# Performance work log

Measured on AMD Instinct MI355X. Metric: run time of the kernel, lower is better.

Reference implementation:

```python
import jax, jax.numpy as jnp
import numpy as np

S = 9                      # spiral length
V = [8192, 4096, 2048, 1024, 512]  # verts per level, finest -> latent


def grid_sample_bilinear(feat, grid):
    # feat [B,C,H,W], grid [B,P,2] in [-1,1]; bilinear, align_corners=True
    B, C, H, W = feat.shape
    x = (grid[..., 0] + 1.0) * 0.5 * (W - 1)
    y = (grid[..., 1] + 1.0) * 0.5 * (H - 1)
    x0 = jnp.floor(x); y0 = jnp.floor(y)
    wx = x - x0; wy = y - y0
    x0i = jnp.clip(x0.astype(jnp.int32), 0, W - 1)
    x1i = jnp.clip(x0.astype(jnp.int32) + 1, 0, W - 1)
    y0i = jnp.clip(y0.astype(jnp.int32), 0, H - 1)
    y1i = jnp.clip(y0.astype(jnp.int32) + 1, 0, H - 1)
    featf = feat.reshape(B, C, H * W).transpose(0, 2, 1)  # [B,HW,C]
    def gat(yi, xi):
        return jnp.take_along_axis(featf, (yi * W + xi)[..., None], axis=1)  # [B,P,C]
    w00 = ((1 - wy) * (1 - wx))[..., None]
    w01 = ((1 - wy) * wx)[..., None]
    w10 = (wy * (1 - wx))[..., None]
    w11 = (wy * wx)[..., None]
    return gat(y0i, x0i) * w00 + gat(y0i, x1i) * w01 + gat(y1i, x0i) * w10 + gat(y1i, x1i) * w11


def pool(x, row, col, val):
    # sparse mesh upsample: gather cols, scale, scatter-add into rows
    n_out = row.shape[0] // 3
    g = x[:, col, :] * val[None, :, None]                       # [B,nnz,C]
    return jnp.zeros((x.shape[0], n_out, x.shape[-1]), x.dtype).at[:, row, :].add(g)


def dsconv(x, idx, wd, wp, b):
    # depthwise-separable spiral conv: gather spiral ring, depthwise over S, pointwise mix
    g = x[:, idx]                                # [B,N,S,C]
    dw = jnp.einsum('bnsc,sc->bnc', g, wd)       # depthwise over spiral dim
    return jnp.einsum('bnc,co->bno', dw, wp) + b # pointwise


def _forward(uv, feat, upsample, s0, s1, s2, s3,
             row0, col0, val0, row1, col1, val1, row2, col2, val2, row3, col3, val3,
             wd0, wp0, b0, wd1, wp1, b1, wd2, wp2, b2, wd3, wp3, b3, wdh, wph, bh):
    uvc = jnp.clip((uv - 0.5) * 2.0, -1.0, 1.0)
    x = grid_sample_bilinear(feat, uvc)           # [B,P,C]  (torch: [B,C,P] then permute)
    x = jnp.einsum('vp,bpc->bvc', upsample, x)    # [B,V4,C] latent mesh features
    x = jax.nn.relu(dsconv(pool(x, row3, col3, val3), s3, wd0, wp0, b0))  # [B,1024,512]
    x = jax.nn.relu(dsconv(pool(x, row2, col2, val2), s2, wd1, wp1, b1))  # [B,2048,256]
    x = jax.nn.relu(dsconv(pool(x, row1, col1, val1), s1, wd2, wp2, b2))  # [B,4096,128]
    x = jax.nn.relu(dsconv(pool(x, row0, col0, val0), s0, wd3, wp3, b3))  # [B,8192,64]
    return dsconv(x, s0, wdh, wph, bh)            # [B,8192,3]


def setup_inputs():
    ks = jax.random.split(jax.random.key(0), 64)
    B, P, C, H, W = 8, 21, 512, 32, 32
    inp = {}
    inp['uv'] = jax.random.uniform(ks[0], (B, P, 2), jnp.float32)
    inp['feat'] = jax.random.normal(ks[1], (B, C, H, W), jnp.float32)
    inp['upsample'] = 0.01 * jnp.ones((V[4], P), jnp.float32)
    for i in range(4):
        inp[f's{i}'] = jax.random.randint(ks[2 + i], (V[i], S), 0, V[i])
    for i in range(4):
        nnz = 3 * V[i]
        inp[f'row{i}'] = jax.random.randint(ks[6 + 3 * i], (nnz,), 0, V[i])
        inp[f'col{i}'] = jax.random.randint(ks[7 + 3 * i], (nnz,), 0, V[i + 1])
        inp[f'val{i}'] = jax.random.uniform(ks[8 + 3 * i], (nnz,), jnp.float32)
    chans = [(512, 512), (512, 256), (256, 128), (128, 64), (64, 3)]
    names = ['0', '1', '2', '3', 'h']
    k = 20
    for (ci, co), nm in zip(chans, names):
        inp[f'wd{nm}'] = 0.1 * jax.random.normal(ks[k], (S, ci), jnp.float32); k += 1
        inp[f'wp{nm}'] = jax.random.normal(ks[k], (ci, co), jnp.float32) * (1.0 / float(np.sqrt(ci))); k += 1
        inp[f'b{nm}'] = jnp.zeros((co,), jnp.float32); k += 1
    return inp


def reference(uv, feat, upsample, s0, s1, s2, s3,
              row0, col0, val0, row1, col1, val1, row2, col2, val2, row3, col3, val3,
              wd0, wp0, b0, wd1, wp1, b1, wd2, wp2, b2, wd3, wp3, b3, wdh, wph, bh):
    return _forward(uv, feat, upsample, s0, s1, s2, s3,
                    row0, col0, val0, row1, col1, val1, row2, col2, val2, row3, col3, val3,
                    wd0, wp0, b0, wd1, wp1, b1, wd2, wp2, b2, wd3, wp3, b3, wdh, wph, bh)
```

## Files before the change

kernel.cpp:

```cpp
#include <hip/hip_runtime.h>

#define B_  8
#define P_  21
#define H_  32
#define W_  32

typedef float f32x4 __attribute__((ext_vector_type(4)));
typedef _Float16 f16x8 __attribute__((ext_vector_type(8)));

__device__ __forceinline__ void gload_lds16(const _Float16* g, _Float16* l) {
  __builtin_amdgcn_global_load_lds(
      (const __attribute__((address_space(1))) void*)g,
      (__attribute__((address_space(3))) void*)l, 16, 0, 0);
}

struct CsrParams {
  const int*   row[4];
  const int*   col[4];
  const float* val[4];
  int*   cnt[4];
  int*   rowptr[4];
  int*   colsout[4];
  float* valsout[4];
  int    nnz[4];
  int    V[4];
};

struct BsplitParams {
  const float* wp[4];
  int K[4], N[4], off[4];
  _Float16* b0;
  _Float16* b1;
};

__global__ __launch_bounds__(256) void k1_zero_sample(
    int* zp, int zn,
    const float* __restrict__ uv,
    const float* __restrict__ feat,
    float* __restrict__ xs) {
  int bid = blockIdx.x;
  if (bid < 60) {
    int i = bid * 256 + threadIdx.x;
    if (i < zn) zp[i] = 0;
    return;
  }
  int bp = bid - 60;
  int b  = bp / P_;
  float u0 = uv[bp * 2 + 0], u1 = uv[bp * 2 + 1];
  float gx = fminf(fmaxf((u0 - 0.5f) * 2.0f, -1.0f), 1.0f);
  float gy = fminf(fmaxf((u1 - 0.5f) * 2.0f, -1.0f), 1.0f);
  float fx = (gx + 1.0f) * 0.5f * (W_ - 1);
  float fy = (gy + 1.0f) * 0.5f * (H_ - 1);
  float x0f = floorf(fx), y0f = floorf(fy);
  float wx = fx - x0f, wy = fy - y0f;
  int x0 = (int)x0f, y0 = (int)y0f;
  int x0i = min(max(x0, 0), W_ - 1), x1i = min(max(x0 + 1, 0), W_ - 1);
  int y0i = min(max(y0, 0), H_ - 1), y1i = min(max(y0 + 1, 0), H_ - 1);
  float w00 = (1.f - wy) * (1.f - wx), w01 = (1.f - wy) * wx;
  float w10 = wy * (1.f - wx),        w11 = wy * wx;
  for (int c = threadIdx.x; c < 512; c += blockDim.x) {
    const float* fb = feat + ((size_t)(b * 512 + c)) * (H_ * W_);
    float v = fb[y0i * W_ + x0i] * w00 + fb[y0i * W_ + x1i] * w01 +
              fb[y1i * W_ + x0i] * w10 + fb[y1i * W_ + x1i] * w11;
    xs[(size_t)bp * 512 + c] = v;
  }
}

__global__ __launch_bounds__(256) void k2_count_upsample(
    CsrParams p,
    const float* __restrict__ up,
    const float* __restrict__ xs,
    float* __restrict__ xu) {
  int bid = blockIdx.x;
  if (bid < 384) {
    int l = bid / 96;
    int k = (bid - l * 96) * 256 + threadIdx.x;
    if (k < p.nnz[l]) atomicAdd(&p.cnt[l][p.row[l][k]], 1);
    return;
  }
  int b2 = bid - 384;
  int b = b2 >> 9, v = b2 & 511;
  int c2 = threadIdx.x << 1;
  float2 acc = make_float2(0.f, 0.f);
  for (int q = 0; q < P_; ++q) {
    float u = up[v * P_ + q];
    const float2 xv = *(const float2*)&xs[((size_t)(b * P_ + q)) * 512 + c2];
    acc.x = fmaf(u, xv.x, acc.x);
    acc.y = fmaf(u, xv.y, acc.y);
  }
  *(float2*)&xu[((size_t)(b * 512 + v)) * 512 + c2] = acc;
}

__global__ __launch_bounds__(256) void k3_scan_bsplit(CsrParams p, BsplitParams bp) {
  int bid = blockIdx.x;
  if (bid < 4) {
    int l = bid;
    int V = p.V[l];
    int* cnt = p.cnt[l];
    int* rp  = p.rowptr[l];
    int t = threadIdx.x;
    int chunk = V / 256;
    int base = t * chunk;
    int s = 0;
    for (int i = 0; i < chunk; ++i) s += cnt[base + i];
    __shared__ int sm[256];
    sm[t] = s;
    __syncthreads();
    for (int off = 1; off < 256; off <<= 1) {
      int v = (t >= off) ? sm[t - off] : 0;
      __syncthreads();
      sm[t] += v;
      __syncthreads();
    }
    int run = sm[t] - s;
    for (int i = 0; i < chunk; ++i) {
      int c = cnt[base + i];
      rp[base + i]  = run;
      cnt[base + i] = run;
      run += c;
    }
    if (t == 255) rp[V] = run;
    return;
  }
  int idx = (bid - 4) * 256 + threadIdx.x;
  #pragma unroll
  for (int t = 0; t < 4; ++t) {
    int sz = bp.N[t] * bp.K[t];
    if (idx < sz) {
      int K = bp.K[t];
      int n = idx / K, k = idx - n * K;
      float v = bp.wp[t][(size_t)k * bp.N[t] + n];
      _Float16 h0 = (_Float16)v;
      float r = (v - (float)h0) * 2048.0f;
      int ks = ((((k >> 3) ^ (n & 7)) << 3) | (k & 7));
      bp.b0[bp.off[t] + (size_t)n * K + ks] = h0;
      bp.b1[bp.off[t] + (size_t)n * K + ks] = (_Float16)r;
      return;
    }
    idx -= sz;
  }
}

__global__ void fill_kernel(CsrParams p) {
  int l = blockIdx.y;
  int k = blockIdx.x * 256 + threadIdx.x;
  if (k < p.nnz[l]) {
    int r = p.row[l][k];
    int pos = atomicAdd(&p.cnt[l][r], 1);
    p.colsout[l][pos] = p.col[l][k];
    p.valsout[l][pos] = p.val[l][k];
  }
}

__global__ __launch_bounds__(256) void pool_kernel(
    const float* __restrict__ x,
    const int* __restrict__ rowptr,
    const int* __restrict__ cols,
    const float* __restrict__ vals,
    float* __restrict__ out,
    int Vout, int Vin, int Cin) {
  const int lpr    = Cin >> 3;
  const int lshift = 31 - __clz(lpr);
  const int rpb    = 256 >> lshift;
  const int lr = threadIdx.x >> lshift;
  const int lc = threadIdx.x & (lpr - 1);
  const int b  = blockIdx.x & 7;
  const int n  = (blockIdx.x >> 3) * rpb + lr;
  const int c8 = lc << 3;
  const float* xb = x + (size_t)b * Vin * Cin + c8;
  int j0 = rowptr[n], j1 = rowptr[n + 1];
  int cnt = j1 - j0;
  float4 a0 = make_float4(0.f, 0.f, 0.f, 0.f);
  float4 a1 = make_float4(0.f, 0.f, 0.f, 0.f);
  if (cnt > 0) {
    int   cc[4];
    float vv[4];
    #pragma unroll
    for (int k = 0; k < 4; ++k) {
      int jj = j0 + ((k < cnt) ? k : 0);
      cc[k] = cols[jj];
      vv[k] = (k < cnt) ? vals[jj] : 0.f;
    }
    #pragma unroll
    for (int k = 0; k < 4; ++k) {
      const float* xr = xb + (size_t)cc[k] * Cin;
      float4 x0 = *(const float4*)xr;
      float4 x1 = *(const float4*)(xr + 4);
      float v = vv[k];
      a0.x = fmaf(v, x0.x, a0.x); a0.y = fmaf(v, x0.y, a0.y);
      a0.z = fmaf(v, x0.z, a0.z); a0.w = fmaf(v, x0.w, a0.w);
      a1.x = fmaf(v, x1.x, a1.x); a1.y = fmaf(v, x1.y, a1.y);
      a1.z = fmaf(v, x1.z, a1.z); a1.w = fmaf(v, x1.w, a1.w);
    }
    for (int j = j0 + 4; j < j1; ++j) {
      float v = vals[j];
      const float* xr = xb + (size_t)cols[j] * Cin;
      float4 x0 = *(const float4*)xr;
      float4 x1 = *(const float4*)(xr + 4);
      a0.x = fmaf(v, x0.x, a0.x); a0.y = fmaf(v, x0.y, a0.y);
      a0.z = fmaf(v, x0.z, a0.z); a0.w = fmaf(v, x0.w, a0.w);
      a1.x = fmaf(v, x1.x, a1.x); a1.y = fmaf(v, x1.y, a1.y);
      a1.z = fmaf(v, x1.z, a1.z); a1.w = fmaf(v, x1.w, a1.w);
    }
  }
  float* op = &out[((size_t)b * Vout + n) * Cin + c8];
  *(float4*)op = a0;
  *(float4*)(op + 4) = a1;
}

__global__ __launch_bounds__(256) void dw_split_kernel(
    const float* __restrict__ xin,
    const int* __restrict__ sidx,
    const float* __restrict__ wd,
    _Float16* __restrict__ a0o,
    _Float16* __restrict__ a1o,
    int Vout, int Cin) {
  const int lpr    = Cin >> 3;
  const int lshift = 31 - __clz(lpr);
  const int rpb    = 256 >> lshift;
  const int lr = threadIdx.x >> lshift;
  const int lc = threadIdx.x & (lpr - 1);
  const int b  = blockIdx.x & 7;
  const int n  = (blockIdx.x >> 3) * rpb + lr;
  const int c8 = lc << 3;
  const float* xb = xin + (size_t)b * Vout * Cin + c8;

  int idx[9];
  #pragma unroll
  for (int s = 0; s < 9; ++s) idx[s] = sidx[n * 9 + s];

  float4 a0 = make_float4(0.f, 0.f, 0.f, 0.f);
  float4 a1 = make_float4(0.f, 0.f, 0.f, 0.f);
  #pragma unroll
  for (int s = 0; s < 9; ++s) {
    const float* xr = xb + (size_t)idx[s] * Cin;
    float4 x0 = *(const float4*)xr;
    float4 x1 = *(const float4*)(xr + 4);
    const float* wr = wd + s * Cin + c8;
    float4 w0 = *(const float4*)wr;
    float4 w1 = *(const float4*)(wr + 4);
    a0.x = fmaf(w0.x, x0.x, a0.x); a0.y = fmaf(w0.y, x0.y, a0.y);
    a0.z = fmaf(w0.z, x0.z, a0.z); a0.w = fmaf(w0.w, x0.w, a0.w);
    a1.x = fmaf(w1.x, x1.x, a1.x); a1.y = fmaf(w1.y, x1.y, a1.y);
    a1.z = fmaf(w1.z, x1.z, a1.z); a1.w = fmaf(w1.w, x1.w, a1.w);
  }

  size_t m = (size_t)b * Vout + n;
  float v[8] = {a0.x, a0.y, a0.z, a0.w, a1.x, a1.y, a1.z, a1.w};
  f16x8 hi, lo;
  #pragma unroll
  for (int i = 0; i < 8; ++i) {
    _Float16 h0 = (_Float16)v[i];
    float r = (v[i] - (float)h0) * 2048.0f;
    hi[i] = h0;
    lo[i] = (_Float16)r;
  }
  const int c8s = (lc ^ (n & 7)) << 3;
  *(f16x8*)&a0o[m * Cin + c8s] = hi;
  *(f16x8*)&a1o[m * Cin + c8s] = lo;
}

__global__ __launch_bounds__(256) void gemm_f16x2(
    const _Float16* __restrict__ A0, const _Float16* __restrict__ A1,
    const _Float16* __restrict__ Bt0, const _Float16* __restrict__ Bt1,
    const float* __restrict__ bias, float* __restrict__ C,
    int M, int N, int K) {
  __shared__ _Float16 As[2][128 * 64];
  __shared__ _Float16 Bs[2][64 * 64];
  const int tid = threadIdx.x;
  const int bx = blockIdx.x;
  const int xr_ = (bx & 7) * (gridDim.x >> 3) + (bx >> 3);
  const int m0 = xr_ * 128, n0 = blockIdx.y * 64;
  const int wid = tid >> 6, lane = tid & 63;
  const int wr = wid >> 1, wc = wid & 1;
  const int lo = lane & 15, hi = lane >> 4;

  f32x4 accM[4][2], accC[4][2];
  #pragma unroll
  for (int mi = 0; mi < 4; ++mi)
    #pragma unroll
    for (int nj = 0; nj < 2; ++nj) {
      accM[mi][nj] = (f32x4){0.f, 0.f, 0.f, 0.f};
      accC[mi][nj] = (f32x4){0.f, 0.f, 0.f, 0.f};
    }

  const _Float16* gA[2] = {A0, A1};
  const _Float16* gB[2] = {Bt0, Bt1};

  for (int k0 = 0; k0 < K; k0 += 64) {
    #pragma unroll
    for (int p = 0; p < 2; ++p) {
      #pragma unroll
      for (int i = 0; i < 4; ++i) {
        int c = tid + 256 * i;
        int r = c >> 3, k8 = (c & 7) << 3;
        gload_lds16(gA[p] + (size_t)(m0 + r) * K + k0 + k8,
                    &As[p][(c & ~63) * 8]);
      }
      #pragma unroll
      for (int i = 0; i < 2; ++i) {
        int c = tid + 256 * i;
        int r = c >> 3, k8 = (c & 7) << 3;
        gload_lds16(gB[p] + (size_t)(n0 + r) * K + k0 + k8,
                    &Bs[p][(c & ~63) * 8]);
      }
    }
    __syncthreads();
    #pragma unroll
    for (int s = 0; s < 2; ++s) {
      const int cl = s * 4 + hi;
      f16x8 af[4][2], bf[2][2];
      #pragma unroll
      for (int mi = 0; mi < 4; ++mi) {
        const int rr = wr * 64 + mi * 16 + lo;
        const int ko = (cl ^ (rr & 7)) << 3;
        af[mi][0] = *(const f16x8*)&As[0][rr * 64 + ko];
        af[mi][1] = *(const f16x8*)&As[1][rr * 64 + ko];
      }
      #pragma unroll
      for (int nj = 0; nj < 2; ++nj) {
        const int rb = wc * 32 + nj * 16 + lo;
        const int ko = (cl ^ (rb & 7)) << 3;
        bf[nj][0] = *(const f16x8*)&Bs[0][rb * 64 + ko];
        bf[nj][1] = *(const f16x8*)&Bs[1][rb * 64 + ko];
      }
      #pragma unroll
      for (int mi = 0; mi < 4; ++mi)
        #pragma unroll
        for (int nj = 0; nj < 2; ++nj) {
          accM[mi][nj] = __builtin_amdgcn_mfma_f32_16x16x32_f16(
              af[mi][0], bf[nj][0], accM[mi][nj], 0, 0, 0);
          accC[mi][nj] = __builtin_amdgcn_mfma_f32_16x16x32_f16(
              af[mi][0], bf[nj][1], accC[mi][nj], 0, 0, 0);
          accC[mi][nj] = __builtin_amdgcn_mfma_f32_16x16x32_f16(
              af[mi][1], bf[nj][0], accC[mi][nj], 0, 0, 0);
        }
    }
    __syncthreads();
  }

  const float INV = 1.0f / 2048.0f;
  #pragma unroll
  for (int mi = 0; mi < 4; ++mi)
    #pragma unroll
    for (int nj = 0; nj < 2; ++nj) {
      int col = n0 + wc * 32 + nj * 16 + lo;
      float bv = bias[col];
      #pragma unroll
      for (int r = 0; r < 4; ++r) {
        int row = m0 + wr * 64 + mi * 16 + hi * 4 + r;
        float v = accM[mi][nj][r] + accC[mi][nj][r] * INV + bv;
        v = fmaxf(v, 0.f);
        C[(size_t)row * N + col] = v;
      }
    }
}

__global__ __launch_bounds__(256) void head_fused_kernel(
    const float* __restrict__ x,
    const int* __restrict__ sidx,
    const float* __restrict__ wdh,
    const float* __restrict__ wph,
    const float* __restrict__ bh,
    float* __restrict__ out) {
  const int bid  = blockIdx.x;
  const int b    = bid & 7;
  const int wid  = threadIdx.x >> 6;
  const int lane = threadIdx.x & 63;
  const int n    = (bid >> 3) * 4 + wid;
  const float* xb = x + (size_t)b * 8192 * 64 + lane;

  int idx[9];
  #pragma unroll
  for (int s = 0; s < 9; ++s) idx[s] = sidx[n * 9 + s];

  float acc = 0.f;
  #pragma unroll
  for (int s = 0; s < 9; ++s)
    acc = fmaf(wdh[s * 64 + lane], xb[(size_t)idx[s] * 64], acc);

  float a0 = acc * wph[lane * 3 + 0];
  float a1 = acc * wph[lane * 3 + 1];
  float a2 = acc * wph[lane * 3 + 2];
  for (int off = 32; off > 0; off >>= 1) {
    a0 += __shfl_down(a0, off);
    a1 += __shfl_down(a1, off);
    a2 += __shfl_down(a2, off);
  }
  if (lane == 0) {
    size_t row = (size_t)b * 8192 + n;
    out[row * 3 + 0] = a0 + bh[0];
    out[row * 3 + 1] = a1 + bh[1];
    out[row * 3 + 2] = a2 + bh[2];
  }
}

extern "C" void kernel_launch(void* const* d_in, const int* in_sizes, int n_in,
                              void* d_out, int out_size, void* d_ws, size_t ws_size,
                              hipStream_t stream) {
  const float* uv   = (const float*)d_in[0];
  const float* feat = (const float*)d_in[1];
  const float* up   = (const float*)d_in[2];
  const int* sArr[4] = {(const int*)d_in[3], (const int*)d_in[4],
                        (const int*)d_in[5], (const int*)d_in[6]};

  const size_t SLAB = 8ull * 2048 * 512;
  float* Wf = (float*)d_ws;
  float* S0 = Wf;
  float* S1 = Wf + SLAB;
  _Float16* A0 = (_Float16*)(S1 + SLAB);
  _Float16* A1 = A0 + SLAB;
  _Float16* Bt0all = (_Float16*)(S0 + 4500000);
  _Float16* Bt1all = Bt0all + 434176;
  float* xs = (float*)(A1 + SLAB);
  int* ib = (int*)(xs + (size_t)B_ * P_ * 512);

  int Vt[4] = {1024, 2048, 4096, 8192};
  int NZ[4] = {3072, 6144, 12288, 24576};
  int* cnt[4]; int* rp[4]; int* co[4]; float* va[4];
  {
    int* pc = ib;
    for (int t = 0; t < 4; ++t) { cnt[t] = pc; pc += Vt[t]; }
    for (int t = 0; t < 4; ++t) { rp[t] = pc; pc += Vt[t] + 1; }
    for (int t = 0; t < 4; ++t) { co[t] = pc; pc += NZ[t]; }
    float* pv = (float*)pc;
    for (int t = 0; t < 4; ++t) { va[t] = pv; pv += NZ[t]; }
  }

  CsrParams cp;
  for (int t = 0; t < 4; ++t) {
    int i = 3 - t;
    cp.row[t] = (const int*)d_in[7 + 3 * i];
    cp.col[t] = (const int*)d_in[8 + 3 * i];
    cp.val[t] = (const float*)d_in[9 + 3 * i];
    cp.cnt[t] = cnt[t]; cp.rowptr[t] = rp[t];
    cp.colsout[t] = co[t]; cp.valsout[t] = va[t];
    cp.nnz[t] = NZ[t]; cp.V[t] = Vt[t];
  }

  struct Stg { int Vin, Vout, Cin, Cout; const int* s; const float *wd, *wp, *bias; };
  Stg st[4] = {
    {512, 1024, 512, 512, sArr[3], (const float*)d_in[19], (const float*)d_in[20], (const float*)d_in[21]},
    {1024, 2048, 512, 256, sArr[2], (const float*)d_in[22], (const float*)d_in[23], (const float*)d_in[24]},
    {2048, 4096, 256, 128, sArr[1], (const float*)d_in[25], (const float*)d_in[26], (const float*)d_in[27]},
    {4096, 8192, 128, 64, sArr[0], (const float*)d_in[28], (const float*)d_in[29], (const float*)d_in[30]},
  };

  BsplitParams bp;
  int boff = 0;
  for (int t = 0; t < 4; ++t) {
    bp.wp[t] = st[t].wp;
    bp.K[t] = st[t].Cin; bp.N[t] = st[t].Cout;
    bp.off[t] = boff;
    boff += st[t].Cin * st[t].Cout;
  }
  bp.b0 = Bt0all; bp.b1 = Bt1all;
  int bsplit_blocks = (boff + 255) / 256;

  k1_zero_sample<<<60 + B_ * P_, 256, 0, stream>>>(ib, 15360, uv, feat, xs);
  k2_count_upsample<<<384 + 512 * B_, 256, 0, stream>>>(cp, up, xs, S0);
  k3_scan_bsplit<<<4 + bsplit_blocks, 256, 0, stream>>>(cp, bp);
  fill_kernel<<<dim3(96, 4), 256, 0, stream>>>(cp);

  for (int t = 0; t < 4; ++t) {
    int rpb = 2048 / st[t].Cin;
    pool_kernel<<<8 * (st[t].Vout / rpb), 256, 0, stream>>>(
        S0, rp[t], co[t], va[t], S1, st[t].Vout, st[t].Vin, st[t].Cin);
    dw_split_kernel<<<8 * (st[t].Vout / rpb), 256, 0, stream>>>(
        S1, st[t].s, st[t].wd, A0, A1, st[t].Vout, st[t].Cin);
    int M = B_ * st[t].Vout;
    gemm_f16x2<<<dim3(M / 128, st[t].Cout / 64), 256, 0, stream>>>(
        A0, A1, Bt0all + bp.off[t], Bt1all + bp.off[t],
        st[t].bias, S0, M, st[t].Cout, st[t].Cin);
  }

  head_fused_kernel<<<8 * (8192 / 4), 256, 0, stream>>>(
      S0, sArr[0], (const float*)d_in[31], (const float*)d_in[32],
      (const float*)d_in[33], (float*)d_out);
}
```

Before: 266.2 us.

## Scalarize row indices, hoist GEMM bias loads, and process two vertices per head wave

Pool and depthwise kernels use readfirstlane on the vertex index when a full wave covers one row, so rowptr and spiral-index loads can become scalar loads. The GEMM loads its bias values before the main K loop rather than in the epilogue. The head kernel now handles two vertices per wave, sharing the depthwise weight loads and halving the block count. The head change roughly doubles per-thread gather and shuffle work in exchange for fewer blocks.

```diff
diff --git a/kernel.cpp b/kernel.cpp
--- a/kernel.cpp
+++ b/kernel.cpp
@@ -168,7 +168,8 @@
   const int n  = (blockIdx.x >> 3) * rpb + lr;
   const int c8 = lc << 3;
   const float* xb = x + (size_t)b * Vin * Cin + c8;
-  int j0 = rowptr[n], j1 = rowptr[n + 1];
+  const int nu = (lpr >= 64) ? __builtin_amdgcn_readfirstlane(n) : n;
+  int j0 = rowptr[nu], j1 = rowptr[nu + 1];
   int cnt = j1 - j0;
   float4 a0 = make_float4(0.f, 0.f, 0.f, 0.f);
   float4 a1 = make_float4(0.f, 0.f, 0.f, 0.f);
@@ -224,10 +225,11 @@
   const int n  = (blockIdx.x >> 3) * rpb + lr;
   const int c8 = lc << 3;
   const float* xb = xin + (size_t)b * Vout * Cin + c8;
+  const int nu = (lpr >= 64) ? __builtin_amdgcn_readfirstlane(n) : n;
 
   int idx[9];
   #pragma unroll
-  for (int s = 0; s < 9; ++s) idx[s] = sidx[n * 9 + s];
+  for (int s = 0; s < 9; ++s) idx[s] = sidx[nu * 9 + s];
 
   float4 a0 = make_float4(0.f, 0.f, 0.f, 0.f);
   float4 a1 = make_float4(0.f, 0.f, 0.f, 0.f);
@@ -274,6 +276,10 @@
   const int wid = tid >> 6, lane = tid & 63;
   const int wr = wid >> 1, wc = wid & 1;
   const int lo = lane & 15, hi = lane >> 4;
+
+  float bv[2];
+  bv[0] = bias[n0 + wc * 32 + 0 * 16 + lo];
+  bv[1] = bias[n0 + wc * 32 + 1 * 16 + lo];
 
   f32x4 accM[4][2], accC[4][2];
   #pragma unroll
@@ -345,11 +351,10 @@
     #pragma unroll
     for (int nj = 0; nj < 2; ++nj) {
       int col = n0 + wc * 32 + nj * 16 + lo;
-      float bv = bias[col];
       #pragma unroll
       for (int r = 0; r < 4; ++r) {
         int row = m0 + wr * 64 + mi * 16 + hi * 4 + r;
-        float v = accM[mi][nj][r] + accC[mi][nj][r] * INV + bv;
+        float v = accM[mi][nj][r] + accC[mi][nj][r] * INV + bv[nj];
         v = fmaxf(v, 0.f);
         C[(size_t)row * N + col] = v;
       }
@@ -367,31 +372,46 @@
   const int b    = bid & 7;
   const int wid  = threadIdx.x >> 6;
   const int lane = threadIdx.x & 63;
-  const int n    = (bid >> 3) * 4 + wid;
+  const int n0   = (bid >> 3) * 8 + wid;
+  const int n1   = n0 + 4;
   const float* xb = x + (size_t)b * 8192 * 64 + lane;
 
-  int idx[9];
-  #pragma unroll
-  for (int s = 0; s < 9; ++s) idx[s] = sidx[n * 9 + s];
-
-  float acc = 0.f;
-  #pragma unroll
-  for (int s = 0; s < 9; ++s)
-    acc = fmaf(wdh[s * 64 + lane], xb[(size_t)idx[s] * 64], acc);
-
-  float a0 = acc * wph[lane * 3 + 0];
-  float a1 = acc * wph[lane * 3 + 1];
-  float a2 = acc * wph[lane * 3 + 2];
+  int idx0[9], idx1[9];
+  #pragma unroll
+  for (int s = 0; s < 9; ++s) idx0[s] = sidx[n0 * 9 + s];
+  #pragma unroll
+  for (int s = 0; s < 9; ++s) idx1[s] = sidx[n1 * 9 + s];
+
+  float acc0 = 0.f, acc1 = 0.f;
+  #pragma unroll
+  for (int s = 0; s < 9; ++s) {
+    float w = wdh[s * 64 + lane];
+    acc0 = fmaf(w, xb[(size_t)idx0[s] * 64], acc0);
+    acc1 = fmaf(w, xb[(size_t)idx1[s] * 64], acc1);
+  }
+
+  float p0 = wph[lane * 3 + 0];
+  float p1 = wph[lane * 3 + 1];
+  float p2 = wph[lane * 3 + 2];
+  float a00 = acc0 * p0, a01 = acc0 * p1, a02 = acc0 * p2;
+  float a10 = acc1 * p0, a11 = acc1 * p1, a12 = acc1 * p2;
   for (int off = 32; off > 0; off >>= 1) {
-    a0 += __shfl_down(a0, off);
-    a1 += __shfl_down(a1, off);
-    a2 += __shfl_down(a2, off);
+    a00 += __shfl_down(a00, off);
+    a01 += __shfl_down(a01, off);
+    a02 += __shfl_down(a02, off);
+    a10 += __shfl_down(a10, off);
+    a11 += __shfl_down(a11, off);
+    a12 += __shfl_down(a12, off);
   }
   if (lane == 0) {
-    size_t row = (size_t)b * 8192 + n;
-    out[row * 3 + 0] = a0 + bh[0];
-    out[row * 3 + 1] = a1 + bh[1];
-    out[row * 3 + 2] = a2 + bh[2];
+    size_t row0 = (size_t)b * 8192 + n0;
+    out[row0 * 3 + 0] = a00 + bh[0];
+    out[row0 * 3 + 1] = a01 + bh[1];
+    out[row0 * 3 + 2] = a02 + bh[2];
+    size_t row1 = (size_t)b * 8192 + n1;
+    out[row1 * 3 + 0] = a10 + bh[0];
+    out[row1 * 3 + 1] = a11 + bh[1];
+    out[row1 * 3 + 2] = a12 + bh[2];
   }
 }
 
@@ -474,7 +494,7 @@
         st[t].bias, S0, M, st[t].Cout, st[t].Cin);
   }
 
-  head_fused_kernel<<<8 * (8192 / 4), 256, 0, stream>>>(
+  head_fused_kernel<<<8 * (8192 / 8), 256, 0, stream>>>(
       S0, sArr[0], (const float*)d_in[31], (const float*)d_in[32],
       (const float*)d_in[33], (float*)d_out);
 }
```

After: 264.3 us. Within noise of the previous version (-0.7%).
